# Optimization experiments

Measured on AMD Instinct MI355X. Metric: run time of the kernel, lower is better.

## Reference

```python
import jax, jax.numpy as jnp
import numpy as np

HIDDEN = 2048
N_HEADS = 16
N_KV_HEADS = 4
HEAD_DIM = 128
GROUPS = N_HEADS // N_KV_HEADS
MAX_SEQ = 2048
EPS = 1e-6
ROTARY_DIM = int(HEAD_DIM * 0.5)  # partial_rotary_factor = 0.5
ROPE_THETA = 10000.0


def _rms_norm(x, w):
    xf = x.astype(jnp.float32)
    normed = xf * jax.lax.rsqrt(jnp.mean(xf * xf, axis=-1, keepdims=True) + EPS)
    return (normed * (1.0 + w.astype(jnp.float32))).astype(x.dtype)


def _apply_rotary(x, cos, sin):
    half = x.shape[-1] // 2
    x1, x2 = x[..., :half], x[..., half:]
    return jnp.concatenate([x1 * cos - x2 * sin, x2 * cos + x1 * sin], axis=-1)


def setup_inputs() -> dict:
    key = jax.random.key(0)
    ks = jax.random.split(key, 6)
    s = 0.02
    return {
        "x": jax.random.normal(ks[0], (1, MAX_SEQ, HIDDEN), jnp.float32),
        "input_pos": jnp.arange(MAX_SEQ, dtype=jnp.int32),
        "wq": jax.random.normal(ks[1], (HIDDEN, N_HEADS * HEAD_DIM * 2), jnp.float32) * s,
        "wk": jax.random.normal(ks[2], (HIDDEN, N_KV_HEADS * HEAD_DIM), jnp.float32) * s,
        "wv": jax.random.normal(ks[3], (HIDDEN, N_KV_HEADS * HEAD_DIM), jnp.float32) * s,
        "wo": jax.random.normal(ks[4], (N_HEADS * HEAD_DIM, HIDDEN), jnp.float32) * s,
        "q_norm_w": jnp.zeros((HEAD_DIM,), jnp.float32),
        "k_norm_w": jnp.zeros((HEAD_DIM,), jnp.float32),
    }


def reference(x, input_pos, wq, wk, wv, wo, q_norm_w, k_norm_w):
    B, T, _ = x.shape
    dtype = x.dtype

    qg = (x @ wq).reshape(B, T, N_HEADS, HEAD_DIM * 2)
    q, gate = qg[..., :HEAD_DIM], qg[..., HEAD_DIM:]
    k = (x @ wk).reshape(B, T, N_KV_HEADS, HEAD_DIM)
    v = (x @ wv).reshape(B, T, N_KV_HEADS, HEAD_DIM)

    q = _rms_norm(q, q_norm_w)
    k = _rms_norm(k, k_norm_w)

    # partial RoPE on the first ROTARY_DIM channels of each head
    inv_freq = 1.0 / ROPE_THETA ** (
        jnp.arange(0, ROTARY_DIM, 2, dtype=jnp.float32) / ROTARY_DIM)
    freqs = jnp.outer(input_pos.astype(jnp.float32), inv_freq)  # [T, rd/2]
    cos = jnp.cos(freqs)[:, None, :]  # [T,1,rd/2] broadcast over heads
    sin = jnp.sin(freqs)[:, None, :]
    q = jnp.concatenate(
        [_apply_rotary(q[..., :ROTARY_DIM], cos, sin), q[..., ROTARY_DIM:]], axis=-1)
    k = jnp.concatenate(
        [_apply_rotary(k[..., :ROTARY_DIM], cos, sin), k[..., ROTARY_DIM:]], axis=-1)

    q = q.astype(dtype).transpose(0, 2, 1, 3)  # [B,H,T,D]
    k = k.astype(dtype).transpose(0, 2, 1, 3)  # [B,Hkv,T,D]
    v = v.transpose(0, 2, 1, 3)

    # KV-cache scatter update (cache starts at zeros)
    kc = jnp.zeros((1, N_KV_HEADS, MAX_SEQ, HEAD_DIM), dtype).at[:, :, input_pos].set(k)
    vc = jnp.zeros((1, N_KV_HEADS, MAX_SEQ, HEAD_DIM), dtype).at[:, :, input_pos].set(v)

    # GQA: group query heads instead of materializing repeated K/V
    qg_ = q.reshape(B, N_KV_HEADS, GROUPS, T, HEAD_DIM)
    scale = 1.0 / jnp.sqrt(jnp.asarray(HEAD_DIM, dtype))
    scores = jnp.einsum("bhgtd,bhsd->bhgts", qg_, kc) * scale  # [B,Hkv,G,T,S]

    mask = jnp.tril(jnp.ones((MAX_SEQ, MAX_SEQ), bool))[input_pos]  # [T,S]
    scores = jnp.where(mask[None, None, None], scores, jnp.finfo(scores.dtype).min)
    probs = jax.nn.softmax(scores, axis=-1)

    y = jnp.einsum("bhgts,bhsd->bhgtd", probs, vc)  # [B,Hkv,G,T,D]
    y = y.reshape(B, N_HEADS, T, HEAD_DIM).transpose(0, 2, 1, 3).reshape(B, T, -1)

    y = y * jax.nn.sigmoid(gate.reshape(B, T, -1))
    return y @ wo
```

## Files before the change

kernel.cpp:

```cpp
#include <hip/hip_runtime.h>
#include <cstdint>
#include <cmath>

using u16 = unsigned short;
typedef __attribute__((ext_vector_type(4))) short s16x4;
typedef __attribute__((ext_vector_type(8))) short s16x8;
typedef __attribute__((ext_vector_type(8))) __bf16 bf16x8;
typedef __attribute__((ext_vector_type(4))) float f32x4;

static __device__ __forceinline__ float b2f(u16 u) {
    unsigned int x = ((unsigned int)u) << 16;
    float f; __builtin_memcpy(&f, &x, 4); return f;
}
static __device__ __forceinline__ u16 f2b(float f) {
    unsigned int x; __builtin_memcpy(&x, &f, 4);
    x += 0x7FFFu + ((x >> 16) & 1u);
    return (u16)(x >> 16);
}
static __device__ __forceinline__ bf16x8 as_bf(s16x8 s) {
    return __builtin_bit_cast(bf16x8, s);
}

static __device__ __forceinline__ void stage16(const u16* g, u16* lds_base, int lane) {
#if __has_builtin(__builtin_amdgcn_global_load_lds)
    __builtin_amdgcn_global_load_lds((const __attribute__((address_space(1))) void*)g,
                                     (__attribute__((address_space(3))) void*)lds_base,
                                     16, 0, 0);
#else
    *(s16x8*)(lds_base + (size_t)lane * 8) = *(const s16x8*)g;
#endif
}

__global__ __launch_bounds__(256) void k_wtransAll(const float* __restrict__ wq,
                                                   const float* __restrict__ wk,
                                                   const float* __restrict__ wv,
                                                   const float* __restrict__ wo,
                                                   u16* __restrict__ wqkvT,
                                                   u16* __restrict__ woT) {
    __shared__ u16 tile[64][72];
    int tx = blockIdx.x;
    const float* src; int N, nb, base; u16* dst;
    if (tx < 64)      { src = wq; N = 4096; nb = tx * 64;        base = tx * 64;               dst = wqkvT; }
    else if (tx < 72) { src = wk; N = 512;  nb = (tx - 64) * 64; base = 4096 + (tx - 64) * 64; dst = wqkvT; }
    else if (tx < 80) { src = wv; N = 512;  nb = (tx - 72) * 64; base = 4608 + (tx - 72) * 64; dst = wqkvT; }
    else              { src = wo; N = 2048; nb = (tx - 80) * 64; base = (tx - 80) * 64;        dst = woT; }
    int kb = blockIdx.y * 64;
    int tid = threadIdx.x;
    int kr = tid >> 2, c0 = (tid & 3) * 16;
#pragma unroll
    for (int i = 0; i < 4; ++i) {
        f32x4 v = *(const f32x4*)(src + (size_t)(kb + kr) * N + nb + c0 + i * 4);
        s16x4 b;
        for (int j = 0; j < 4; ++j) b[j] = (short)f2b(v[j]);
        *(s16x4*)&tile[kr][c0 + i * 4] = b;
    }
    __syncthreads();
    int nr = tid >> 2, k0 = (tid & 3) * 16;
    s16x8 v0, v1;
    for (int j = 0; j < 8; ++j) { v0[j] = (short)tile[k0 + j][nr]; v1[j] = (short)tile[k0 + 8 + j][nr]; }
    *(s16x8*)(dst + (size_t)(base + nr) * 2048 + kb + k0) = v0;
    *(s16x8*)(dst + (size_t)(base + nr) * 2048 + kb + k0 + 8) = v1;
}

__global__ __launch_bounds__(256) void k_xcvt(const float* __restrict__ in,
                                              u16* __restrict__ out, int n4) {
    int i = blockIdx.x * 256 + threadIdx.x;
    int stride = gridDim.x * 256;
    for (; i < n4; i += stride) {
        f32x4 v = ((const f32x4*)in)[i];
        s16x4 b;
        for (int j = 0; j < 4; ++j) b[j] = (short)f2b(v[j]);
        ((s16x4*)out)[i] = b;
    }
}

template <bool OUT_F32>
__global__ __launch_bounds__(256) void k_gemm_bt(const u16* __restrict__ A,
                                                 const u16* __restrict__ Bt,
                                                 void* __restrict__ Cv,
                                                 int M, int N, int K) {
    __shared__ u16 As[128 * 64];
    __shared__ u16 Bs[128 * 64];
    int nx = gridDim.x, ny = gridDim.y;
    int flat = blockIdx.y * nx + blockIdx.x;
    int xcd = flat & 7, i = flat >> 3;
    int P = nx >> 3;
    int bnl = i / ny;
    int bmi = i - bnl * ny;
    if (bnl & 1) bmi = ny - 1 - bmi;
    int bn = (xcd * P + bnl) * 128;
    int bm = bmi * 128;

    int tid = threadIdx.x, wid = tid >> 6, lane = tid & 63;
    int l15 = lane & 15, g = lane >> 4;
    int wr = (wid >> 1) * 64, wc = (wid & 1) * 64;
    f32x4 acc[4][4];
    for (int ii = 0; ii < 4; ++ii) for (int j = 0; j < 4; ++j) acc[ii][j] = f32x4{0.f, 0.f, 0.f, 0.f};

    int srow = lane >> 3;
    int scol = ((lane & 7) * 8) ^ (srow << 3);
    const u16* pa = A + (size_t)(bm + srow) * K + scol;
    const u16* pb = Bt + (size_t)(bn + srow) * K + scol;

    for (int kb = 0; kb < K; kb += 64) {
        __syncthreads();
#pragma unroll
        for (int it = 0; it < 4; ++it) {
            int c = it * 4 + wid;
            stage16(pa + (size_t)(c * 8) * K + kb, &As[c * 512], lane);
            stage16(pb + (size_t)(c * 8) * K + kb, &Bs[c * 512], lane);
        }
        __syncthreads();
        int swz = (l15 & 7) << 4;
#pragma unroll
        for (int kk = 0; kk < 64; kk += 32) {
            bf16x8 af[4], bfr[4];
            for (int mi = 0; mi < 4; ++mi) {
                const char* rp = (const char*)As + (wr + mi * 16 + l15) * 128;
                af[mi] = as_bf(*(const s16x8*)(rp + ((kk * 2 + g * 16) ^ swz)));
            }
            for (int ni = 0; ni < 4; ++ni) {
                const char* rp = (const char*)Bs + (wc + ni * 16 + l15) * 128;
                bfr[ni] = as_bf(*(const s16x8*)(rp + ((kk * 2 + g * 16) ^ swz)));
            }
            for (int mi = 0; mi < 4; ++mi)
                for (int ni = 0; ni < 4; ++ni)
                    acc[mi][ni] = __builtin_amdgcn_mfma_f32_16x16x32_bf16(af[mi], bfr[ni], acc[mi][ni], 0, 0, 0);
        }
    }
    for (int mi = 0; mi < 4; ++mi)
        for (int ni = 0; ni < 4; ++ni) {
            int row = bm + wr + mi * 16 + g * 4;
            int col = bn + wc + ni * 16 + l15;
            for (int rr = 0; rr < 4; ++rr) {
                if (OUT_F32)
                    ((float*)Cv)[(size_t)(row + rr) * N + col] = acc[mi][ni][rr];
                else
                    ((u16*)Cv)[(size_t)(row + rr) * N + col] = f2b(acc[mi][ni][rr]);
            }
        }
}

__global__ __launch_bounds__(256) void k_prep_attn(u16* __restrict__ qkv,
                                                   const float* __restrict__ qw,
                                                   const float* __restrict__ kw,
                                                   const int* __restrict__ pos,
                                                   u16* __restrict__ vT) {
    __shared__ u16 tile[64][136];
    int bid = blockIdx.x;
    int tid = threadIdx.x;
    if (bid < 2048) {
        int t = bid, w = tid >> 6, l = tid & 63;
        float fp = (float)pos[t];
        int j = l & 31;
        float invf = __expf(-(float)j * (9.210340371976184f / 32.f));
        float sv, cv;
        sincosf(fp * invf, &sv, &cv);
        for (int task = w; task < 20; task += 4) {
            u16* p; const float* ww;
            if (task < 16) { p = qkv + (size_t)t * 5120 + task * 256; ww = qw; }
            else           { p = qkv + (size_t)t * 5120 + 4096 + (task - 16) * 128; ww = kw; }
            float v0 = b2f(p[l]), v1 = b2f(p[l + 64]);
            float ss = v0 * v0 + v1 * v1;
            for (int m = 32; m; m >>= 1) ss += __shfl_xor(ss, m);
            float rn = rsqrtf(ss * (1.f / 128.f) + 1e-6f);
            float q0 = v0 * rn * (1.f + ww[l]);
            float q1 = v1 * rn * (1.f + ww[l + 64]);
            float other = __shfl_xor(q0, 32);
            float ro = (l < 32) ? (q0 * cv - other * sv) : (q0 * cv + other * sv);
            p[l] = f2b(ro);
            p[l + 64] = f2b(q1);
        }
    } else {
        int r = bid - 2048;
        int tb = (r & 31) * 64, kvh = r >> 5;
        int tr = tid >> 2, c0 = (tid & 3) * 32;
        const u16* src = qkv + (size_t)(tb + tr) * 5120 + 4608 + kvh * 128 + c0;
#pragma unroll
        for (int i = 0; i < 4; ++i)
            *(s16x8*)&tile[tr][c0 + i * 8] = *(const s16x8*)(src + i * 8);
        __syncthreads();
        int d = tid >> 1, t0 = (tid & 1) * 32;
        u16* dst = vT + ((size_t)kvh * 128 + d) * 2048 + tb + t0;
#pragma unroll
        for (int i = 0; i < 4; ++i) {
            s16x8 v;
            for (int j = 0; j < 8; ++j) v[j] = (short)tile[t0 + i * 8 + j][d];
            *(s16x8*)(dst + i * 8) = v;
        }
    }
}

__global__ __launch_bounds__(256) void k_attn_split(const u16* __restrict__ qkv,
                                                    const u16* __restrict__ vT,
                                                    u16* __restrict__ po,
                                                    float* __restrict__ pl) {
    __shared__ u16 Kl[64 * 128];
    __shared__ u16 Vt[128][72];
    __shared__ u16 Pl[4][16][72];
    int head = blockIdx.y, kvh = head >> 2;
    int p = blockIdx.x / 3, hf = blockIdx.x % 3;
    int tid = threadIdx.x, wid = tid >> 6, lane = tid & 63;
    int l15 = lane & 15, g = lane >> 4;

    for (int sub = 0; sub < 2; ++sub) {
        int qt = sub ? (31 - p) : p;
        int qb0 = qt * 64;
        int nk_all = qt + 1;
        int ktb = (hf * nk_all) / 3;
        int kte = ((hf + 1) * nk_all) / 3;

        bf16x8 qf[4];
        {
            const u16* qp = qkv + (size_t)(qb0 + wid * 16 + l15) * 5120 + head * 256 + g * 8;
            for (int c = 0; c < 4; ++c) qf[c] = as_bf(*(const s16x8*)(qp + c * 32));
        }
        f32x4 oacc[8];
        for (int nb = 0; nb < 8; ++nb) oacc[nb] = f32x4{0.f, 0.f, 0.f, 0.f};
        float lsum[4] = {0.f, 0.f, 0.f, 0.f};

        for (int kt = ktb; kt < kte; ++kt) {
            int k0 = kt * 64;
            __syncthreads();
            {
#pragma unroll
                for (int i = 0; i < 4; ++i) {
                    int c = (wid << 2) | i;
                    int srow = (c << 2) + (lane >> 4);
                    int bofs = (((lane & 15) << 4) ^ ((srow & 7) << 4));
                    const u16* gs = (const u16*)((const char*)(qkv + (size_t)(k0 + srow) * 5120
                                                               + 4096 + kvh * 128) + bofs);
                    stage16(gs, &Kl[c * 512], lane);
                }
                int vr = tid >> 1, vc0 = (tid & 1) * 32;
                const u16* vs = vT + ((size_t)kvh * 128 + vr) * 2048 + k0 + vc0;
#pragma unroll
                for (int c = 0; c < 4; ++c)
                    *(s16x8*)&Vt[vr][vc0 + 8 * c] = *(const s16x8*)(vs + 8 * c);
            }
            __syncthreads();

            f32x4 sc4[4];
            for (int h2 = 0; h2 < 4; ++h2) sc4[h2] = f32x4{0.f, 0.f, 0.f, 0.f};
            for (int h2 = 0; h2 < 4; ++h2) {
                int krow = h2 * 16 + l15;
                const char* kb_ = (const char*)Kl + krow * 256;
                int sw = (krow & 7) << 4;
                for (int c = 0; c < 4; ++c) {
                    bf16x8 kf = as_bf(*(const s16x8*)(kb_ + ((c * 64 + g * 16) ^ sw)));
                    sc4[h2] = __builtin_amdgcn_mfma_f32_16x16x32_bf16(qf[c], kf, sc4[h2], 0, 0, 0);
                }
            }
            const float scale = 0.08838834764831845f;
            for (int r = 0; r < 4; ++r) {
                int tq = qb0 + wid * 16 + g * 4 + r;
                float prs = 0.f;
                for (int h2 = 0; h2 < 4; ++h2) {
                    bool msk = (k0 + h2 * 16 + l15) > tq;
                    float pv = msk ? 0.f : __expf(sc4[h2][r] * scale);
                    prs += pv;
                    Pl[wid][g * 4 + r][h2 * 16 + l15] = f2b(pv);
                }
                lsum[r] += prs;
            }
            for (int kc = 0; kc < 2; ++kc) {
                bf16x8 pa = as_bf(*(const s16x8*)&Pl[wid][l15][kc * 32 + g * 8]);
                for (int nb = 0; nb < 8; ++nb) {
                    bf16x8 vb = as_bf(*(const s16x8*)&Vt[nb * 16 + l15][kc * 32 + g * 8]);
                    oacc[nb] = __builtin_amdgcn_mfma_f32_16x16x32_bf16(pa, vb, oacc[nb], 0, 0, 0);
                }
            }
        }
        u16* pob = po + (size_t)hf * (2048 * 2048);
        float* plb = pl + hf * (16 * 2048) + head * 2048;
        for (int r = 0; r < 4; ++r) {
            float s = lsum[r];
            s += __shfl_xor(s, 1, 16); s += __shfl_xor(s, 2, 16);
            s += __shfl_xor(s, 4, 16); s += __shfl_xor(s, 8, 16);
            int row = qb0 + wid * 16 + g * 4 + r;
            if (l15 == 0) plb[row] = s;
            for (int nb = 0; nb < 8; ++nb)
                pob[(size_t)row * 2048 + head * 128 + nb * 16 + l15] = f2b(oacc[nb][r]);
        }
    }
}

__global__ __launch_bounds__(256) void k_combine(u16* __restrict__ po,
                                                 const float* __restrict__ pl,
                                                 const u16* __restrict__ qkv) {
    int t = blockIdx.x;
    int tid = threadIdx.x;
    int h = tid >> 4, d0 = (tid & 15) * 8;
    const size_t S = (size_t)2048 * 2048;
    const size_t base = (size_t)t * 2048 + h * 128 + d0;
    s16x8 a = *(const s16x8*)(po + base);
    s16x8 b = *(const s16x8*)(po + S + base);
    s16x8 c = *(const s16x8*)(po + 2 * S + base);
    int li = h * 2048 + t;
    float l = pl[li] + pl[16 * 2048 + li] + pl[32 * 2048 + li];
    float inv = 1.f / l;
    s16x8 o;
    for (int j = 0; j < 8; ++j) {
        float y = (b2f((u16)a[j]) + b2f((u16)b[j]) + b2f((u16)c[j])) * inv;
        float gt = b2f(qkv[(size_t)t * 5120 + h * 256 + 128 + d0 + j]);
        o[j] = (short)f2b(y / (1.f + __expf(-gt)));
    }
    *(s16x8*)(po + base) = o;
}

extern "C" void kernel_launch(void* const* d_in, const int* in_sizes, int n_in,
                              void* d_out, int out_size, void* d_ws, size_t ws_size,
                              hipStream_t stream) {
    const float* x   = (const float*)d_in[0];
    const int*   pos = (const int*)d_in[1];
    const float* wq  = (const float*)d_in[2];
    const float* wk  = (const float*)d_in[3];
    const float* wv  = (const float*)d_in[4];
    const float* wo  = (const float*)d_in[5];
    const float* qnw = (const float*)d_in[6];
    const float* knw = (const float*)d_in[7];
    float* out = (float*)d_out;
    char* ws = (char*)d_ws;

    u16*   qkv   = (u16*)(ws + 0);
    u16*   woT   = (u16*)(ws + 20971520);
    u16*   wqkvT = (u16*)(ws + 29360128);
    u16*   xb    = (u16*)(ws + 50331648);
    u16*   vTb   = (u16*)(ws + 29360128);
    u16*   pob   = (u16*)(ws + 31457280);
    float* plb   = (float*)(ws + 56623104);

    k_wtransAll<<<dim3(112, 32), 256, 0, stream>>>(wq, wk, wv, wo, wqkvT, woT);
    k_xcvt<<<1024, 256, 0, stream>>>(x, xb, 2048 * 2048 / 4);

    k_gemm_bt<false><<<dim3(40, 16), 256, 0, stream>>>(xb, wqkvT, qkv, 2048, 5120, 2048);

    k_prep_attn<<<2176, 256, 0, stream>>>(qkv, qnw, knw, pos, vTb);

    k_attn_split<<<dim3(48, 16), 256, 0, stream>>>(qkv, vTb, pob, plb);
    k_combine<<<2048, 256, 0, stream>>>(pob, plb, qkv);

    k_gemm_bt<true><<<dim3(16, 16), 256, 0, stream>>>(pob, woT, out, 2048, 2048, 2048);
}
```

Baseline: 177.7 us.

## Split attention KV into four parts with 32-key tiles and fuse x conversion

The attention kernel now splits each query tile's key range into four parts instead of three and processes keys in 32-wide tiles, raising the grid to 1024 blocks for better load balance. The combine kernel sums four partial outputs and denominators, and the workspace layout is shifted to hold the extra partial buffer. The separate fp32-to-bf16 conversion of x is folded into the weight transpose launch as extra blocks, removing one kernel launch. The smaller key tiles double the barrier count per key and the combine reads more partial data.

```diff
diff --git a/kernel.cpp b/kernel.cpp
--- a/kernel.cpp
+++ b/kernel.cpp
@@ -35,17 +35,32 @@
                                                    const float* __restrict__ wk,
                                                    const float* __restrict__ wv,
                                                    const float* __restrict__ wo,
+                                                   const float* __restrict__ x,
                                                    u16* __restrict__ wqkvT,
-                                                   u16* __restrict__ woT) {
+                                                   u16* __restrict__ woT,
+                                                   u16* __restrict__ xb) {
     __shared__ u16 tile[64][72];
     int tx = blockIdx.x;
+    int tid = threadIdx.x;
+    if (tx >= 112) {
+        int bid = (tx - 112) * 32 + blockIdx.y;
+        int i = bid * 256 + tid;
+        const int n4 = 2048 * 2048 / 4;
+        const int stride = 1024 * 256;
+        for (; i < n4; i += stride) {
+            f32x4 v = ((const f32x4*)x)[i];
+            s16x4 b;
+            for (int j = 0; j < 4; ++j) b[j] = (short)f2b(v[j]);
+            ((s16x4*)xb)[i] = b;
+        }
+        return;
+    }
     const float* src; int N, nb, base; u16* dst;
     if (tx < 64)      { src = wq; N = 4096; nb = tx * 64;        base = tx * 64;               dst = wqkvT; }
     else if (tx < 72) { src = wk; N = 512;  nb = (tx - 64) * 64; base = 4096 + (tx - 64) * 64; dst = wqkvT; }
     else if (tx < 80) { src = wv; N = 512;  nb = (tx - 72) * 64; base = 4608 + (tx - 72) * 64; dst = wqkvT; }
     else              { src = wo; N = 2048; nb = (tx - 80) * 64; base = (tx - 80) * 64;        dst = woT; }
     int kb = blockIdx.y * 64;
-    int tid = threadIdx.x;
     int kr = tid >> 2, c0 = (tid & 3) * 16;
 #pragma unroll
     for (int i = 0; i < 4; ++i) {
@@ -60,18 +75,6 @@
     for (int j = 0; j < 8; ++j) { v0[j] = (short)tile[k0 + j][nr]; v1[j] = (short)tile[k0 + 8 + j][nr]; }
     *(s16x8*)(dst + (size_t)(base + nr) * 2048 + kb + k0) = v0;
     *(s16x8*)(dst + (size_t)(base + nr) * 2048 + kb + k0 + 8) = v1;
-}
-
-__global__ __launch_bounds__(256) void k_xcvt(const float* __restrict__ in,
-                                              u16* __restrict__ out, int n4) {
-    int i = blockIdx.x * 256 + threadIdx.x;
-    int stride = gridDim.x * 256;
-    for (; i < n4; i += stride) {
-        f32x4 v = ((const f32x4*)in)[i];
-        s16x4 b;
-        for (int j = 0; j < 4; ++j) b[j] = (short)f2b(v[j]);
-        ((s16x4*)out)[i] = b;
-    }
 }
 
 template <bool OUT_F32>
@@ -195,20 +198,20 @@
                                                     const u16* __restrict__ vT,
                                                     u16* __restrict__ po,
                                                     float* __restrict__ pl) {
-    __shared__ u16 Kl[64 * 128];
+    __shared__ u16 Kl[32 * 128];
     __shared__ u16 Vt[128][72];
-    __shared__ u16 Pl[4][16][72];
+    __shared__ u16 Pl[4][16][40];
     int head = blockIdx.y, kvh = head >> 2;
-    int p = blockIdx.x / 3, hf = blockIdx.x % 3;
+    int p = blockIdx.x >> 2, hf = blockIdx.x & 3;
     int tid = threadIdx.x, wid = tid >> 6, lane = tid & 63;
     int l15 = lane & 15, g = lane >> 4;
 
     for (int sub = 0; sub < 2; ++sub) {
         int qt = sub ? (31 - p) : p;
         int qb0 = qt * 64;
-        int nk_all = qt + 1;
-        int ktb = (hf * nk_all) / 3;
-        int kte = ((hf + 1) * nk_all) / 3;
+        int nk = (qt + 1) * 2;
+        int ktb = (hf * nk) >> 2;
+        int kte = ((hf + 1) * nk) >> 2;
 
         bf16x8 qf[4];
         {
@@ -220,55 +223,50 @@
         float lsum[4] = {0.f, 0.f, 0.f, 0.f};
 
         for (int kt = ktb; kt < kte; ++kt) {
-            int k0 = kt * 64;
+            int k0 = kt * 32;
             __syncthreads();
             {
 #pragma unroll
-                for (int i = 0; i < 4; ++i) {
-                    int c = (wid << 2) | i;
+                for (int i = 0; i < 2; ++i) {
+                    int c = (wid << 1) | i;
                     int srow = (c << 2) + (lane >> 4);
                     int bofs = (((lane & 15) << 4) ^ ((srow & 7) << 4));
                     const u16* gs = (const u16*)((const char*)(qkv + (size_t)(k0 + srow) * 5120
                                                                + 4096 + kvh * 128) + bofs);
                     stage16(gs, &Kl[c * 512], lane);
                 }
-                int vr = tid >> 1, vc0 = (tid & 1) * 32;
+                int vr = tid >> 1, vc0 = (tid & 1) * 16;
                 const u16* vs = vT + ((size_t)kvh * 128 + vr) * 2048 + k0 + vc0;
 #pragma unroll
-                for (int c = 0; c < 4; ++c)
+                for (int c = 0; c < 2; ++c)
                     *(s16x8*)&Vt[vr][vc0 + 8 * c] = *(const s16x8*)(vs + 8 * c);
             }
             __syncthreads();
 
-            f32x4 sc4[4];
-            for (int h2 = 0; h2 < 4; ++h2) sc4[h2] = f32x4{0.f, 0.f, 0.f, 0.f};
-            for (int h2 = 0; h2 < 4; ++h2) {
+            f32x4 sc2[2];
+            sc2[0] = f32x4{0.f, 0.f, 0.f, 0.f}; sc2[1] = f32x4{0.f, 0.f, 0.f, 0.f};
+            for (int h2 = 0; h2 < 2; ++h2) {
                 int krow = h2 * 16 + l15;
                 const char* kb_ = (const char*)Kl + krow * 256;
                 int sw = (krow & 7) << 4;
                 for (int c = 0; c < 4; ++c) {
                     bf16x8 kf = as_bf(*(const s16x8*)(kb_ + ((c * 64 + g * 16) ^ sw)));
-                    sc4[h2] = __builtin_amdgcn_mfma_f32_16x16x32_bf16(qf[c], kf, sc4[h2], 0, 0, 0);
+                    sc2[h2] = __builtin_amdgcn_mfma_f32_16x16x32_bf16(qf[c], kf, sc2[h2], 0, 0, 0);
                 }
             }
             const float scale = 0.08838834764831845f;
             for (int r = 0; r < 4; ++r) {
                 int tq = qb0 + wid * 16 + g * 4 + r;
-                float prs = 0.f;
-                for (int h2 = 0; h2 < 4; ++h2) {
-                    bool msk = (k0 + h2 * 16 + l15) > tq;
-                    float pv = msk ? 0.f : __expf(sc4[h2][r] * scale);
-                    prs += pv;
-                    Pl[wid][g * 4 + r][h2 * 16 + l15] = f2b(pv);
-                }
-                lsum[r] += prs;
-            }
-            for (int kc = 0; kc < 2; ++kc) {
-                bf16x8 pa = as_bf(*(const s16x8*)&Pl[wid][l15][kc * 32 + g * 8]);
-                for (int nb = 0; nb < 8; ++nb) {
-                    bf16x8 vb = as_bf(*(const s16x8*)&Vt[nb * 16 + l15][kc * 32 + g * 8]);
-                    oacc[nb] = __builtin_amdgcn_mfma_f32_16x16x32_bf16(pa, vb, oacc[nb], 0, 0, 0);
-                }
+                float pv0 = (k0 + l15 > tq) ? 0.f : __expf(sc2[0][r] * scale);
+                float pv1 = (k0 + 16 + l15 > tq) ? 0.f : __expf(sc2[1][r] * scale);
+                Pl[wid][g * 4 + r][l15] = f2b(pv0);
+                Pl[wid][g * 4 + r][16 + l15] = f2b(pv1);
+                lsum[r] += pv0 + pv1;
+            }
+            bf16x8 pa = as_bf(*(const s16x8*)&Pl[wid][l15][g * 8]);
+            for (int nb = 0; nb < 8; ++nb) {
+                bf16x8 vb = as_bf(*(const s16x8*)&Vt[nb * 16 + l15][g * 8]);
+                oacc[nb] = __builtin_amdgcn_mfma_f32_16x16x32_bf16(pa, vb, oacc[nb], 0, 0, 0);
             }
         }
         u16* pob = po + (size_t)hf * (2048 * 2048);
@@ -296,12 +294,13 @@
     s16x8 a = *(const s16x8*)(po + base);
     s16x8 b = *(const s16x8*)(po + S + base);
     s16x8 c = *(const s16x8*)(po + 2 * S + base);
+    s16x8 d = *(const s16x8*)(po + 3 * S + base);
     int li = h * 2048 + t;
-    float l = pl[li] + pl[16 * 2048 + li] + pl[32 * 2048 + li];
+    float l = pl[li] + pl[16 * 2048 + li] + pl[32 * 2048 + li] + pl[48 * 2048 + li];
     float inv = 1.f / l;
     s16x8 o;
     for (int j = 0; j < 8; ++j) {
-        float y = (b2f((u16)a[j]) + b2f((u16)b[j]) + b2f((u16)c[j])) * inv;
+        float y = (b2f((u16)a[j]) + b2f((u16)b[j]) + b2f((u16)c[j]) + b2f((u16)d[j])) * inv;
         float gt = b2f(qkv[(size_t)t * 5120 + h * 256 + 128 + d0 + j]);
         o[j] = (short)f2b(y / (1.f + __expf(-gt)));
     }
@@ -328,16 +327,15 @@
     u16*   xb    = (u16*)(ws + 50331648);
     u16*   vTb   = (u16*)(ws + 29360128);
     u16*   pob   = (u16*)(ws + 31457280);
-    float* plb   = (float*)(ws + 56623104);
-
-    k_wtransAll<<<dim3(112, 32), 256, 0, stream>>>(wq, wk, wv, wo, wqkvT, woT);
-    k_xcvt<<<1024, 256, 0, stream>>>(x, xb, 2048 * 2048 / 4);
+    float* plb   = (float*)(ws + 65011712);
+
+    k_wtransAll<<<dim3(144, 32), 256, 0, stream>>>(wq, wk, wv, wo, x, wqkvT, woT, xb);
 
     k_gemm_bt<false><<<dim3(40, 16), 256, 0, stream>>>(xb, wqkvT, qkv, 2048, 5120, 2048);
 
     k_prep_attn<<<2176, 256, 0, stream>>>(qkv, qnw, knw, pos, vTb);
 
-    k_attn_split<<<dim3(48, 16), 256, 0, stream>>>(qkv, vTb, pob, plb);
+    k_attn_split<<<dim3(64, 16), 256, 0, stream>>>(qkv, vTb, pob, plb);
     k_combine<<<2048, 256, 0, stream>>>(pob, plb, qkv);
 
     k_gemm_bt<true><<<dim3(16, 16), 256, 0, stream>>>(pob, woT, out, 2048, 2048, 2048);
```

Result: no change. 174.9 us (median of 2 runs) (-1.6%).
